# Performance work log

Measured on AMD Instinct MI355X. Metric: run time of the kernel, lower is better.

Reference implementation:

```python
import jax, jax.numpy as jnp
import numpy as np

B, S, F, H, T = 1024, 64, 2, 128, 24  # batch, src_len, n_features, hidden, output_length


def setup_inputs() -> dict:
    key = jax.random.key(0)
    ks = jax.random.split(key, 20)
    def p(k, shape):
        return jax.random.normal(k, shape, jnp.float32) * 0.05
    return {
        "x": jax.random.normal(ks[0], (B, S, F), jnp.float32),
        "prev_y": jnp.zeros((B, F), jnp.float32),
        # encoder 3-layer LSTM (PyTorch gate order i,f,g,o; b = b_ih + b_hh fused)
        "enc_Wih0": p(ks[1], (4 * H, F)),
        "enc_Whh0": p(ks[2], (4 * H, H)),
        "enc_b0": p(ks[3], (4 * H,)),
        "enc_Wih12": p(ks[4], (2, 4 * H, H)),
        "enc_Whh12": p(ks[5], (2, 4 * H, H)),
        "enc_b12": p(ks[6], (2, 4 * H)),
        # Bahdanau attention
        "attn_W": p(ks[7], (H, 2 * H)),
        "attn_b": p(ks[8], (H,)),
        "v_W": p(ks[9], (H,)),
        # decoder 3-layer LSTM, input size H+2
        "dec_Wih0": p(ks[10], (4 * H, H + 2)),
        "dec_Whh0": p(ks[11], (4 * H, H)),
        "dec_b0": p(ks[12], (4 * H,)),
        "dec_Wih12": p(ks[13], (2, 4 * H, H)),
        "dec_Whh12": p(ks[14], (2, 4 * H, H)),
        "dec_b12": p(ks[15], (2, 4 * H)),
        # output head Linear(2H, 2)
        "out_W": p(ks[16], (2, 2 * H)),
        "out_b": p(ks[17], (2,)),
    }


def _lstm_cell(xt, h, c, Wih, Whh, b):
    g = xt @ Wih.T + h @ Whh.T + b  # [B, 4H]
    i, f, gg, o = jnp.split(g, 4, axis=-1)
    c = jax.nn.sigmoid(f) * c + jax.nn.sigmoid(i) * jnp.tanh(gg)
    h = jax.nn.sigmoid(o) * jnp.tanh(c)
    return h, c


def _lstm_layer(xs, Wih, Whh, b):
    # xs: [S, B, in] -> hs [S, B, H], final (h, c)
    z = jnp.zeros((xs.shape[1], Whh.shape[1]), xs.dtype)
    def step(carry, xt):
        h, c = _lstm_cell(xt, carry[0], carry[1], Wih, Whh, b)
        return (h, c), h
    (hT, cT), hs = jax.lax.scan(step, (z, z), xs)
    return hs, hT, cT


def reference(x, prev_y, enc_Wih0, enc_Whh0, enc_b0, enc_Wih12, enc_Whh12, enc_b12,
              attn_W, attn_b, v_W, dec_Wih0, dec_Whh0, dec_b0, dec_Wih12, dec_Whh12,
              dec_b12, out_W, out_b):
    # ---- encoder: 3-layer LSTM over time ----
    hs, h0, c0 = _lstm_layer(jnp.swapaxes(x, 0, 1), enc_Wih0, enc_Whh0, enc_b0)
    hid, cel = [h0], [c0]
    for l in range(2):
        hs, hT, cT = _lstm_layer(hs, enc_Wih12[l], enc_Whh12[l], enc_b12[l])
        hid.append(hT); cel.append(cT)
    enc_out = jnp.swapaxes(hs, 0, 1)            # [B, S, H]
    h = jnp.stack(hid)                           # [3, B, H]
    c = jnp.stack(cel)

    def dec_step(carry, _):
        prev_out, h, c = carry
        h_top = h[2]                                             # top-layer hidden [B, H]
        a_in = jnp.concatenate(
            [jnp.broadcast_to(h_top[:, None, :], enc_out.shape), enc_out], axis=-1)  # [B, S, 2H]
        scores = jnp.tanh(a_in @ attn_W.T + attn_b) @ v_W        # [B, S]
        attw = jax.nn.softmax(scores, axis=1)
        weighted = jnp.einsum('bs,bsd->bd', attw, enc_out)        # [B, H]
        rnn_in = jnp.concatenate([prev_out, weighted], axis=-1)   # [B, H+2]
        h0n, c0n = _lstm_cell(rnn_in, h[0], c[0], dec_Wih0, dec_Whh0, dec_b0)
        h1n, c1n = _lstm_cell(h0n, h[1], c[1], dec_Wih12[0], dec_Whh12[0], dec_b12[0])
        h2n, c2n = _lstm_cell(h1n, h[2], c[2], dec_Wih12[1], dec_Whh12[1], dec_b12[1])
        out = jnp.concatenate([h2n, weighted], axis=-1) @ out_W.T + out_b  # [B, 2]
        return (out, jnp.stack([h0n, h1n, h2n]), jnp.stack([c0n, c1n, c2n])), out

    _, outs = jax.lax.scan(dec_step, (prev_y, h, c), None, length=T)
    return outs  # [T, B, 2]
```

## Files before the change

### kernel.cpp

```cpp
#include <hip/hip_runtime.h>
#include <hip/hip_fp16.h>

#define SEQ   64
#define HID   128
#define TOUT  24

typedef unsigned int u32;
typedef _Float16 f16;
typedef __attribute__((ext_vector_type(8))) f16 f16x8;
typedef __attribute__((ext_vector_type(4))) float f32x4;
#define MFMA __builtin_amdgcn_mfma_f32_16x16x32_f16

static __device__ __forceinline__ float sigm(float x){
  return __builtin_amdgcn_rcpf(1.f + __expf(-x));
}
static __device__ __forceinline__ float tanh_fast(float x){
  return fmaf(2.f, __builtin_amdgcn_rcpf(1.f + __expf(-2.f*x)), -1.f);
}

__global__ void prep_kernel(
    const float* __restrict__ eWih0,  const float* __restrict__ eWhh0,
    const float* __restrict__ eWih12, const float* __restrict__ eWhh12,
    const float* __restrict__ aW,
    const float* __restrict__ dWih0,  const float* __restrict__ dWhh0,
    const float* __restrict__ dWih12, const float* __restrict__ dWhh12,
    const float* __restrict__ oW,
    __half* __restrict__ wE0, __half* __restrict__ wE1, __half* __restrict__ wE2,
    __half* __restrict__ wD0, __half* __restrict__ wD1, __half* __restrict__ wD2,
    __half* __restrict__ wAh, __half* __restrict__ wAeF, float* __restrict__ wOT,
    float* __restrict__ dW2)
{
  int id = blockIdx.x*blockDim.x + threadIdx.x;
  if (id < 65536){
    int m=id, jj=m&7, l=(m>>3)&63, kt=(m>>9)&3, nt=m>>11;
    int col = nt*16 + (l&15), k = kt*32 + ((l>>4)<<3) + jj;
    wE0[m] = __float2half(eWhh0[col*128 + k]); return;
  }
  id -= 65536;
  if (id < 5*131072){
    int seg = id >> 17, m = id & 131071;
    int jj=m&7, l=(m>>3)&63, kt=(m>>9)&7, nt=m>>12;
    int col = nt*16 + (l&15), k = kt*32 + ((l>>4)<<3) + jj;
    float v;
    if (seg==0)      v = (k<128)? eWih12[col*128+k]         : eWhh12[col*128 + (k-128)];
    else if (seg==1) v = (k<128)? eWih12[65536+col*128+k]   : eWhh12[65536 + col*128 + (k-128)];
    else if (seg==2) v = (k<128)? dWih0[col*130 + 2 + k]    : dWhh0[col*128 + (k-128)];
    else if (seg==3) v = (k<128)? dWih12[col*128+k]         : dWhh12[col*128 + (k-128)];
    else             v = (k<128)? dWih12[65536+col*128+k]   : dWhh12[65536 + col*128 + (k-128)];
    __half hv = __float2half(v);
    if (seg==0){ wE1[m] = hv; return; }
    if (seg==1){ wE2[m] = hv; return; }
    __half* dst = (seg==2)? wD0 : (seg==3)? wD1 : wD2;
#pragma unroll
    for (int c=0; c<4; ++c) dst[(size_t)c*131072 + m] = hv;
    return;
  }
  id -= 5*131072;
  if (id < 16384){
    int m=id, jj=m&7, l=(m>>3)&63, kt=(m>>9)&3, nt=m>>11;
    int col = nt*16 + (l&15), k = kt*32 + ((l>>4)<<3) + jj;
    __half hv = __float2half(aW[col*256 + k]);
#pragma unroll
    for (int c=0; c<4; ++c) wAh[(size_t)c*16384 + m] = hv;
    return;
  }
  id -= 16384;
  if (id < 16384){
    int m=id, jj=m&7, l=(m>>3)&63, kt=(m>>9)&3, nt=m>>11;
    int col = nt*16 + (l&15), k = kt*32 + ((l>>4)<<3) + jj;
    wAeF[m] = __float2half(aW[col*256 + 128 + k]); return;
  }
  id -= 16384;
  if (id < 512){ int k=id>>1, jo=id&1; wOT[id] = oW[jo*256 + k]; return; }
  id -= 512;
  if (id < 1024){ int col=id>>1, ki=id&1; dW2[id] = dWih0[col*130 + ki]; return; }
}

__global__ __launch_bounds__(512) __attribute__((amdgpu_waves_per_eu(2, 2)))
void enc_kernel(
    const float* __restrict__ x, const float* __restrict__ eb0,
    const float* __restrict__ eb12, const float* __restrict__ eWih0,
    const __half* __restrict__ wE0, const __half* __restrict__ wE1,
    const __half* __restrict__ wE2,
    __half* __restrict__ hs0, __half* __restrict__ hs1,
    __half* __restrict__ carryH, float* __restrict__ carryC)
{
  __shared__ __align__(16) __half hT[2][2048];

  const int tid = threadIdx.x, w = tid>>6, lane = tid&63;
  const int l15 = lane&15, g4 = lane>>4;
  const int j = w*16 + l15;
  const int b16 = blockIdx.x*16;
  const int K0 = ((j>>5)*64 + ((j>>3)&3)*16)*8 + (j&7);

  __half* hs0b = hs0 + (size_t)blockIdx.x*131072;
  __half* hs1b = hs1 + (size_t)blockIdx.x*131072;

  for (int layer=0; layer<3; ++layer){
    const __half* W  = (layer==0)? wE0 : (layer==1)? wE1 : wE2;
    const float* bs  = (layer==0)? eb0 : (layer==1)? eb12 : (eb12+512);
    const __half* hinb  = (layer==1)? hs0b : hs1b;
    __half* houtb = (layer==0)? hs0b : (layer==1)? hs1b : nullptr;

    float bias[4];
#pragma unroll
    for (int g=0; g<4; ++g) bias[g] = bs[g*128 + j];
    float2 wx[4];
    if (layer==0){
#pragma unroll
      for (int g=0; g<4; ++g) wx[g] = *(const float2*)(eWih0 + (g*128+j)*2);
    }
    const f16x8* wb = (const f16x8*)W + lane;
    f16x8 Wh[16];
    if (layer==0){
#pragma unroll
      for (int g=0; g<4; ++g)
#pragma unroll
        for (int kt=0; kt<4; ++kt) Wh[g*4+kt] = wb[(size_t)((g*8+w)*4 + kt)*64];
    } else {
#pragma unroll
      for (int g=0; g<4; ++g)
#pragma unroll
        for (int kt=0; kt<4; ++kt) Wh[g*4+kt] = wb[(size_t)((g*8+w)*8 + 4 + kt)*64];
    }
    float c[4] = {0.f,0.f,0.f,0.f};
    ((u32*)hT[0])[tid] = 0u; ((u32*)hT[0])[tid+512] = 0u;
    __syncthreads();

    float2 xv[4]; f16x8 alo[4];
    if (layer==0){
#pragma unroll
      for (int q=0; q<4; ++q) xv[q] = *(const float2*)(x + ((size_t)(b16+g4*4+q)*SEQ + 0)*2);
    } else {
#pragma unroll
      for (int kt=0; kt<4; ++kt) alo[kt] = *(const f16x8*)(hinb + (kt*64+lane)*8);
    }

    int cur = 0;
    for (int t=0; t<SEQ; ++t){
      f16x8 wi[16];
      if (layer>0){
#pragma unroll
        for (int g=0; g<4; ++g)
#pragma unroll
          for (int kt=0; kt<4; ++kt) wi[g*4+kt] = wb[(size_t)((g*8+w)*8 + kt)*64];
      }
      f16x8 ah[4];
#pragma unroll
      for (int kt=0; kt<4; ++kt) ah[kt] = *(const f16x8*)(hT[cur] + (kt*64+lane)*8);
      float2 xcur[4]; f16x8 acur[4];
      if (layer==0){
#pragma unroll
        for (int q=0; q<4; ++q) xcur[q] = xv[q];
        if (t+1 < SEQ)
#pragma unroll
          for (int q=0; q<4; ++q) xv[q] = *(const float2*)(x + ((size_t)(b16+g4*4+q)*SEQ + t+1)*2);
      } else {
#pragma unroll
        for (int kt=0; kt<4; ++kt) acur[kt] = alo[kt];
        if (t+1 < SEQ)
#pragma unroll
          for (int kt=0; kt<4; ++kt) alo[kt] = *(const f16x8*)(hinb + (size_t)(t+1)*2048 + (kt*64+lane)*8);
      }
      f32x4 acc[4];
#pragma unroll
      for (int g=0; g<4; ++g) acc[g] = (f32x4){0.f,0.f,0.f,0.f};
#pragma unroll
      for (int g=0; g<4; ++g)
#pragma unroll
        for (int kt=0; kt<4; ++kt) acc[g] = MFMA(ah[kt], Wh[g*4+kt], acc[g], 0,0,0);
      if (layer>0){
#pragma unroll
        for (int g=0; g<4; ++g)
#pragma unroll
          for (int kt=0; kt<4; ++kt) acc[g] = MFMA(acur[kt], wi[g*4+kt], acc[g], 0,0,0);
      }
#pragma unroll
      for (int q=0; q<4; ++q){
        float gi = acc[0][q]+bias[0], gf = acc[1][q]+bias[1],
              gg = acc[2][q]+bias[2], go = acc[3][q]+bias[3];
        if (layer==0){
          gi += xcur[q].x*wx[0].x + xcur[q].y*wx[0].y;
          gf += xcur[q].x*wx[1].x + xcur[q].y*wx[1].y;
          gg += xcur[q].x*wx[2].x + xcur[q].y*wx[2].y;
          go += xcur[q].x*wx[3].x + xcur[q].y*wx[3].y;
        }
        float cn = fmaf(sigm(gf), c[q], sigm(gi)*tanh_fast(gg));
        float hn = sigm(go)*tanh_fast(cn);
        c[q] = cn;
        __half hh = __float2half(hn);
        hT[cur^1][K0 + (g4*4+q)*8] = hh;
        if (layer < 2){
          houtb[(size_t)t*2048 + K0 + (g4*4+q)*8] = hh;
        } else {
          int off = g4*32768 + q*8192 + (t>>4)*2048 + (j>>5)*512
                  + ((t&15) + ((j>>3)&3)*16)*8 + (j&7);
          hs0b[off] = hh;
        }
        if (t == SEQ-1){
          int ci = (layer*1024 + b16 + g4*4 + q)*128 + j;
          carryH[ci] = hh;
          carryC[ci] = cn;
        }
      }
      __syncthreads();
      cur ^= 1;
    }
    __syncthreads();
  }
}

#define LDQ(Q, g, kh) \
  Q[0] = wb[(size_t)((g)*64 + (kh)*4 + 0)*64]; \
  Q[1] = wb[(size_t)((g)*64 + (kh)*4 + 1)*64]; \
  Q[2] = wb[(size_t)((g)*64 + (kh)*4 + 2)*64]; \
  Q[3] = wb[(size_t)((g)*64 + (kh)*4 + 3)*64];
#define MM4(Q, A, g) \
  acc[g] = MFMA(A[0], Q[0], acc[g], 0,0,0); \
  acc[g] = MFMA(A[1], Q[1], acc[g], 0,0,0); \
  acc[g] = MFMA(A[2], Q[2], acc[g], 0,0,0); \
  acc[g] = MFMA(A[3], Q[3], acc[g], 0,0,0);

static __device__ __forceinline__ void dec_gemm(const __half* __restrict__ W,
    const __half* __restrict__ A0, const __half* __restrict__ A1,
    f32x4* acc, int lane, int w8)
{
  const f16x8* wb = (const f16x8*)W + (size_t)(w8*8)*64 + lane;
  f16x8 qA[4], qB[4], a0[4], a1[4];
  LDQ(qA, 0, 0)
  LDQ(qB, 1, 0)
#pragma unroll
  for (int kt=0; kt<4; ++kt) a0[kt] = *(const f16x8*)(A0 + (kt*64+lane)*8);
#pragma unroll
  for (int g=0; g<4; ++g) acc[g] = (f32x4){0.f,0.f,0.f,0.f};
  MM4(qA, a0, 0)  LDQ(qA, 2, 0)
  MM4(qB, a0, 1)  LDQ(qB, 3, 0)
#pragma unroll
  for (int kt=0; kt<4; ++kt) a1[kt] = *(const f16x8*)(A1 + (kt*64+lane)*8);
  MM4(qA, a0, 2)  LDQ(qA, 0, 1)
  MM4(qB, a0, 3)  LDQ(qB, 1, 1)
  MM4(qA, a1, 0)  LDQ(qA, 2, 1)
  MM4(qB, a1, 1)  LDQ(qB, 3, 1)
  MM4(qA, a1, 2)
  MM4(qB, a1, 3)
}

__global__ __launch_bounds__(512)
void dec_kernel(
    const float* __restrict__ prev_y, const float* __restrict__ db0,
    const float* __restrict__ db12, const float* __restrict__ ob,
    const float* __restrict__ ab, const float* __restrict__ vW,
    const __half* __restrict__ wD0, const __half* __restrict__ wD1,
    const __half* __restrict__ wD2, const __half* __restrict__ wAh,
    const __half* __restrict__ wAeF, const float* __restrict__ wOT,
    const float* __restrict__ dW2, const __half* __restrict__ encAg,
    const __half* __restrict__ carryH, const float* __restrict__ carryC,
    float* __restrict__ dout)
{
  __shared__ __align__(16) __half hT[4][2048];
  __shared__ float hp[4][132];
  __shared__ float scbF[256];
  __shared__ __align__(16) __half scb16h[256];
  __shared__ float po[4][2];
  __shared__ float vwl[128];
  extern __shared__ __align__(16) __half dyn[];
  __half* encBL = dyn;
  __half* epL   = dyn + 32768;

  const int tid = threadIdx.x, w = tid>>6, lane = tid&63;
  const int l15 = lane&15, g4 = lane>>4;
  const int d = blockIdx.x, b4 = d*4;
  const int w8 = (w + d) & 7;
  const int j = w8*16 + l15;
  const int K0 = ((j>>5)*64 + ((j>>3)&3)*16)*8 + (j&7);
  const __half* encAd = encAg + (size_t)(d>>2)*131072 + (size_t)(d&3)*32768;
  const int cp = (d>>3)&3;
  const __half* wD0d = wD0 + (size_t)cp*131072;
  const __half* wD1d = wD1 + (size_t)cp*131072;
  const __half* wD2d = wD2 + (size_t)cp*131072;
  const __half* wAhd = wAh + (size_t)cp*16384;

  float cD[3][4];
  if (g4 == 0){
#pragma unroll
    for (int l=0; l<3; ++l)
#pragma unroll
      for (int q=0; q<4; ++q){
        int ci = (l*1024 + b4 + q)*128 + j;
        hT[1+l][K0 + q*8] = carryH[ci];
        cD[l][q] = carryC[ci];
      }
  }
  if (tid < 8) po[tid>>1][tid&1] = prev_y[(b4 + (tid>>1))*2 + (tid&1)];
  if (tid < 128) vwl[tid] = vW[tid];

#pragma unroll
  for (int it=0; it<8; ++it){
    int lin = it*512 + tid;
    f16x8 v = *(const f16x8*)(encAd + (size_t)lin*8);
    int laneA = lin&63, ktA = (lin>>6)&3, sb = (lin>>8)&3, r4 = (lin>>10)&3;
    int s  = sb*16 + (laneA&15);
    int d0 = ktA*32 + ((laneA>>4)<<3);
    int base = r4*8192 + ((d0>>4)*2 + (s>>5))*512 + (s&7);
    int lb0  = (d0&15) + ((s>>3)&3)*16;
    f16* eb = (f16*)encBL;
#pragma unroll
    for (int u=0; u<8; ++u) eb[base + (lb0+u)*8] = v[u];
  }
#pragma unroll
  for (int i=0; i<2; ++i){
    int mt = w*2 + i, r4 = mt>>2, sb = mt&3;
    f16x8 a[4];
#pragma unroll
    for (int kt=0; kt<4; ++kt)
      a[kt] = *(const f16x8*)(encAd + (size_t)(((r4*4+sb)*4 + kt)*64 + lane)*8);
    const f16x8* bw = (const f16x8*)wAeF + lane;
#pragma unroll
    for (int nt=0; nt<8; ++nt){
      int col = nt*16 + l15;
      float abv = ab[col];
      f32x4 acc = {abv, abv, abv, abv};
#pragma unroll
      for (int kt=0; kt<4; ++kt) acc = MFMA(a[kt], bw[(size_t)(nt*4+kt)*64], acc, 0,0,0);
      int srow = r4*64 + sb*16 + g4*4;
#pragma unroll
      for (int q=0; q<4; ++q) epL[(srow+q)*132 + col] = __float2half(acc[q]);
    }
  }
  __syncthreads();

  auto cell = [&](float* crl, const float* bdp, const float* dwp, __half* hdst,
                  const f32x4* acc){
    float b0 = bdp[j], b1 = bdp[128+j], b2 = bdp[256+j], b3 = bdp[384+j];
    float2 w0, w1, w2, w3;
    if (dwp){
      w0 = *(const float2*)(dwp + 2*j);
      w1 = *(const float2*)(dwp + 2*(128+j));
      w2 = *(const float2*)(dwp + 2*(256+j));
      w3 = *(const float2*)(dwp + 2*(384+j));
    }
#pragma unroll
    for (int q=0; q<4; ++q){
      float gi = acc[0][q]+b0, gf = acc[1][q]+b1, gg = acc[2][q]+b2, go = acc[3][q]+b3;
      if (dwp){
        float p0 = po[q][0], p1 = po[q][1];
        gi += p0*w0.x + p1*w0.y;
        gf += p0*w1.x + p1*w1.y;
        gg += p0*w2.x + p1*w2.y;
        go += p0*w3.x + p1*w3.y;
      }
      float cn = fmaf(sigm(gf), crl[q], sigm(gi)*tanh_fast(gg));
      float hn = sigm(go)*tanh_fast(cn);
      crl[q] = cn;
      hdst[K0 + q*8] = __float2half(hn);
    }
  };

  int zr = 0;
  for (int t=0; t<TOUT; ++t){
    asm volatile("" : "+v"(zr));
    const float*  db0t  = db0  + zr;
    const float*  db12t = db12 + zr;
    const float*  dW2t  = dW2  + zr;
    const __half* wAht  = wAhd + zr;

    {
      f16x8 a[4], wAhR[4];
      const f16x8* wbh = (const f16x8*)wAht + lane;
#pragma unroll
      for (int kt=0; kt<4; ++kt) wAhR[kt] = wbh[(size_t)(w8*4+kt)*64];
#pragma unroll
      for (int kt=0; kt<4; ++kt) a[kt] = *(const f16x8*)(hT[3] + (kt*64+lane)*8);
      f32x4 acc = {0.f,0.f,0.f,0.f};
#pragma unroll
      for (int kt=0; kt<4; ++kt) acc = MFMA(a[kt], wAhR[kt], acc, 0,0,0);
      if (g4 == 0){
#pragma unroll
        for (int q=0; q<4; ++q) hp[q][j] = acc[q];
      }
    }
    __syncthreads();
    {
      int rs = tid>>1, r = rs>>6, jh = tid&1;
      const __half* er = epL + rs*132 + jh*64;
      const float* hr = hp[r] + jh*64;
      const float* vr = vwl + jh*64;
      float sc = 0.f;
#pragma unroll
      for (int p=0; p<8; ++p){
        f16x8 e = *(const f16x8*)(er + p*8);
#pragma unroll
        for (int u=0; u<8; ++u)
          sc = fmaf(tanh_fast((float)e[u] + hr[p*8+u]), vr[p*8+u], sc);
      }
      sc += __shfl_xor(sc, 1);
      if (jh == 0) scbF[rs] = sc;
    }
    __syncthreads();
    if (tid < 256){
      float v = scbF[tid];
      float m = v;
#pragma unroll
      for (int off=32; off; off>>=1) m = fmaxf(m, __shfl_xor(m, off));
      float e = __expf(v - m);
      float sm = e;
#pragma unroll
      for (int off=32; off; off>>=1) sm += __shfl_xor(sm, off);
      scb16h[tid] = __float2half(e * __builtin_amdgcn_rcpf(sm));
    }
    __syncthreads();
    {
#pragma unroll
      for (int r=0; r<4; ++r){
        f32x4 acc = {0.f,0.f,0.f,0.f};
#pragma unroll
        for (int kt=0; kt<2; ++kt){
          f16x8 abc = *(const f16x8*)(scb16h + r*64 + kt*32 + g4*8);
          f16x8 b   = *(const f16x8*)(encBL + r*8192 + ((w8*2+kt)*64 + lane)*8);
          acc = MFMA(abc, b, acc, 0,0,0);
        }
        if (lane < 16) hT[0][K0 + r*8] = __float2half(acc[0]);
      }
    }
    __syncthreads();
    f32x4 acc[4];
    dec_gemm(wD0d, hT[0], hT[1], acc, lane, w8);
    if (g4 == 0) cell(cD[0], db0t, dW2t, hT[1], acc);
    __syncthreads();
    dec_gemm(wD1d, hT[1], hT[2], acc, lane, w8);
    if (g4 == 0) cell(cD[1], db12t, nullptr, hT[2], acc);
    __syncthreads();
    dec_gemm(wD2d, hT[2], hT[3], acc, lane, w8);
    if (g4 == 0) cell(cD[2], db12t + 512, nullptr, hT[3], acc);
    __syncthreads();
    if (tid < 256){
      int r = tid>>6, kl = tid&63;
      int k2 = kl*2;
      int sl = ((k2>>5)*64 + r + ((k2>>3)&3)*16)*8 + (k2&7);
      float2 h2f = __half22float2(*(const __half2*)(hT[3] + sl));
      float2 wwf = __half22float2(*(const __half2*)(hT[0] + sl));
      float2 a0 = *(const float2*)(wOT + k2*2);
      float2 a1 = *(const float2*)(wOT + k2*2 + 2);
      float2 b0v = *(const float2*)(wOT + (128+k2)*2);
      float2 b1v = *(const float2*)(wOT + (128+k2)*2 + 2);
      float o0 = h2f.x*a0.x + h2f.y*a1.x + wwf.x*b0v.x + wwf.y*b1v.x;
      float o1 = h2f.x*a0.y + h2f.y*a1.y + wwf.x*b0v.y + wwf.y*b1v.y;
#pragma unroll
      for (int off=32; off; off>>=1){ o0 += __shfl_xor(o0, off); o1 += __shfl_xor(o1, off); }
      if (kl == 0){
        float v0 = o0 + ob[0], v1 = o1 + ob[1];
        size_t oi = ((size_t)t*1024 + b4 + r)*2;
        dout[oi] = v0; dout[oi+1] = v1;
        po[r][0] = v0; po[r][1] = v1;
      }
    }
  }
}

extern "C" void kernel_launch(void* const* d_in, const int* in_sizes, int n_in,
                              void* d_out, int out_size, void* d_ws, size_t ws_size,
                              hipStream_t stream) {
  const float* x      = (const float*)d_in[0];
  const float* prev_y = (const float*)d_in[1];
  const float* eWih0  = (const float*)d_in[2];
  const float* eWhh0  = (const float*)d_in[3];
  const float* eb0    = (const float*)d_in[4];
  const float* eWih12 = (const float*)d_in[5];
  const float* eWhh12 = (const float*)d_in[6];
  const float* eb12   = (const float*)d_in[7];
  const float* aW     = (const float*)d_in[8];
  const float* ab     = (const float*)d_in[9];
  const float* vW     = (const float*)d_in[10];
  const float* dWih0  = (const float*)d_in[11];
  const float* dWhh0  = (const float*)d_in[12];
  const float* db0    = (const float*)d_in[13];
  const float* dWih12 = (const float*)d_in[14];
  const float* dWhh12 = (const float*)d_in[15];
  const float* db12   = (const float*)d_in[16];
  const float* oW     = (const float*)d_in[17];
  const float* ob     = (const float*)d_in[18];

  __half* wE0  = (__half*)d_ws;
  __half* wE1  = wE0 + 65536;
  __half* wE2  = wE1 + 131072;
  __half* wD0  = wE2 + 131072;
  __half* wD1  = wD0 + 4*131072;
  __half* wD2  = wD1 + 4*131072;
  __half* wAh  = wD2 + 4*131072;
  __half* wAeF = wAh + 4*16384;
  float*  wOT  = (float*)(wAeF + 16384);
  float*  dW2  = wOT + 512;
  __half* hs0  = (__half*)(dW2 + 1024);
  __half* hs1  = hs0 + (size_t)64*131072;
  __half* carryH = hs1 + (size_t)64*131072;
  float*  carryC = (float*)(carryH + 393216);

  const int prepN = 65536 + 5*131072 + 16384 + 16384 + 512 + 1024;
  prep_kernel<<<(prepN + 255)/256, 256, 0, stream>>>(
      eWih0, eWhh0, eWih12, eWhh12, aW, dWih0, dWhh0, dWih12, dWhh12, oW,
      wE0, wE1, wE2, wD0, wD1, wD2, wAh, wAeF, wOT, dW2);

  enc_kernel<<<64, 512, 0, stream>>>(
      x, eb0, eb12, eWih0, wE0, wE1, wE2, hs0, hs1, carryH, carryC);

  const int dynB = (32768 + 256*132) * 2;
  hipFuncSetAttribute(reinterpret_cast<const void*>(dec_kernel),
                      hipFuncAttributeMaxDynamicSharedMemorySize, dynB);
  dec_kernel<<<256, 512, dynB, stream>>>(
      prev_y, db0, db12, ob, ab, vW, wD0, wD1, wD2, wAh, wAeF, wOT, dW2,
      hs0, carryH, carryC, (float*)d_out);
}
```

Baseline: 749.7 us.

## Split encoder gates across 16 waves and stage gate preactivations in LDS

The encoder now launches 1024 threads per block instead of 512. Each wave computes two 16-column gate tiles, keeps both the recurrent and input weight fragments in registers, and writes preactivations to shared memory. A barrier follows, then each thread applies the LSTM cell for two hidden units of one batch row. This is meant to halve the per-wave MFMA chain length and stop reloading input weights from global memory every timestep, at the cost of an extra barrier and an LDS round trip per step. Separately, the decoder weight copies are reduced from four replicas to two, which cuts prep-kernel writes but may increase cache contention in the decoder.

New measurement: 686.3 us. -8.5%, faster.

```diff
diff --git a/kernel.cpp b/kernel.cpp
--- a/kernel.cpp
+++ b/kernel.cpp
@@ -51,8 +51,7 @@
     if (seg==0){ wE1[m] = hv; return; }
     if (seg==1){ wE2[m] = hv; return; }
     __half* dst = (seg==2)? wD0 : (seg==3)? wD1 : wD2;
-#pragma unroll
-    for (int c=0; c<4; ++c) dst[(size_t)c*131072 + m] = hv;
+    dst[m] = hv; dst[131072 + m] = hv;
     return;
   }
   id -= 5*131072;
@@ -60,8 +59,7 @@
     int m=id, jj=m&7, l=(m>>3)&63, kt=(m>>9)&3, nt=m>>11;
     int col = nt*16 + (l&15), k = kt*32 + ((l>>4)<<3) + jj;
     __half hv = __float2half(aW[col*256 + k]);
-#pragma unroll
-    for (int c=0; c<4; ++c) wAh[(size_t)c*16384 + m] = hv;
+    wAh[m] = hv; wAh[16384 + m] = hv;
     return;
   }
   id -= 16384;
@@ -76,8 +74,7 @@
   if (id < 1024){ int col=id>>1, ki=id&1; dW2[id] = dWih0[col*130 + ki]; return; }
 }
 
-__global__ __launch_bounds__(512) __attribute__((amdgpu_waves_per_eu(2, 2)))
-void enc_kernel(
+__global__ __launch_bounds__(1024) void enc_kernel(
     const float* __restrict__ x, const float* __restrict__ eb0,
     const float* __restrict__ eb12, const float* __restrict__ eWih0,
     const __half* __restrict__ wE0, const __half* __restrict__ wE1,
@@ -86,12 +83,14 @@
     __half* __restrict__ carryH, float* __restrict__ carryC)
 {
   __shared__ __align__(16) __half hT[2][2048];
+  __shared__ __align__(16) float gpre[16*516];
+  __shared__ float xc[2][16][2];
 
   const int tid = threadIdx.x, w = tid>>6, lane = tid&63;
   const int l15 = lane&15, g4 = lane>>4;
-  const int j = w*16 + l15;
   const int b16 = blockIdx.x*16;
-  const int K0 = ((j>>5)*64 + ((j>>3)&3)*16)*8 + (j&7);
+  const int rp = tid>>6;
+  const int c0 = tid&63;
 
   __half* hs0b = hs0 + (size_t)blockIdx.x*131072;
   __half* hs1b = hs1 + (size_t)blockIdx.x*131072;
@@ -99,106 +98,106 @@
   for (int layer=0; layer<3; ++layer){
     const __half* W  = (layer==0)? wE0 : (layer==1)? wE1 : wE2;
     const float* bs  = (layer==0)? eb0 : (layer==1)? eb12 : (eb12+512);
-    const __half* hinb  = (layer==1)? hs0b : hs1b;
+    const __half* hinb = (layer==1)? hs0b : hs1b;
     __half* houtb = (layer==0)? hs0b : (layer==1)? hs1b : nullptr;
 
-    float bias[4];
-#pragma unroll
-    for (int g=0; g<4; ++g) bias[g] = bs[g*128 + j];
-    float2 wx[4];
+    float bias[4][2];
+#pragma unroll
+    for (int g=0; g<4; ++g){
+      bias[g][0] = bs[g*128 + c0];
+      bias[g][1] = bs[g*128 + c0 + 64];
+    }
+    float2 wx[4][2];
     if (layer==0){
 #pragma unroll
-      for (int g=0; g<4; ++g) wx[g] = *(const float2*)(eWih0 + (g*128+j)*2);
+      for (int g=0; g<4; ++g){
+        wx[g][0] = *(const float2*)(eWih0 + (g*128 + c0)*2);
+        wx[g][1] = *(const float2*)(eWih0 + (g*128 + c0 + 64)*2);
+      }
     }
     const f16x8* wb = (const f16x8*)W + lane;
-    f16x8 Wh[16];
+    f16x8 Wh[2][4], Wi[2][4];
     if (layer==0){
 #pragma unroll
-      for (int g=0; g<4; ++g)
-#pragma unroll
-        for (int kt=0; kt<4; ++kt) Wh[g*4+kt] = wb[(size_t)((g*8+w)*4 + kt)*64];
+      for (int n2=0; n2<2; ++n2)
+#pragma unroll
+        for (int kt=0; kt<4; ++kt) Wh[n2][kt] = wb[(size_t)((2*w+n2)*4 + kt)*64];
     } else {
 #pragma unroll
-      for (int g=0; g<4; ++g)
-#pragma unroll
-        for (int kt=0; kt<4; ++kt) Wh[g*4+kt] = wb[(size_t)((g*8+w)*8 + 4 + kt)*64];
-    }
-    float c[4] = {0.f,0.f,0.f,0.f};
-    ((u32*)hT[0])[tid] = 0u; ((u32*)hT[0])[tid+512] = 0u;
-    __syncthreads();
-
-    float2 xv[4]; f16x8 alo[4];
-    if (layer==0){
-#pragma unroll
-      for (int q=0; q<4; ++q) xv[q] = *(const float2*)(x + ((size_t)(b16+g4*4+q)*SEQ + 0)*2);
-    } else {
-#pragma unroll
-      for (int kt=0; kt<4; ++kt) alo[kt] = *(const f16x8*)(hinb + (kt*64+lane)*8);
-    }
+      for (int n2=0; n2<2; ++n2)
+#pragma unroll
+        for (int kt=0; kt<4; ++kt){
+          Wh[n2][kt] = wb[(size_t)((2*w+n2)*8 + 4 + kt)*64];
+          Wi[n2][kt] = wb[(size_t)((2*w+n2)*8 + kt)*64];
+        }
+    }
+    float c2[2] = {0.f, 0.f};
+    ((u32*)hT[0])[tid] = 0u;
+    if (layer==0 && tid < 32)
+      xc[0][tid>>1][tid&1] = x[((size_t)(b16 + (tid>>1))*SEQ + 0)*2 + (tid&1)];
+    __syncthreads();
 
     int cur = 0;
     for (int t=0; t<SEQ; ++t){
-      f16x8 wi[16];
+      f16x8 ah[4];
+#pragma unroll
+      for (int kt=0; kt<4; ++kt) ah[kt] = *(const f16x8*)(hT[cur] + (kt*64+lane)*8);
+      f32x4 acc[2];
+#pragma unroll
+      for (int n2=0; n2<2; ++n2) acc[n2] = (f32x4){0.f,0.f,0.f,0.f};
+#pragma unroll
+      for (int n2=0; n2<2; ++n2)
+#pragma unroll
+        for (int kt=0; kt<4; ++kt) acc[n2] = MFMA(ah[kt], Wh[n2][kt], acc[n2], 0,0,0);
       if (layer>0){
-#pragma unroll
-        for (int g=0; g<4; ++g)
-#pragma unroll
-          for (int kt=0; kt<4; ++kt) wi[g*4+kt] = wb[(size_t)((g*8+w)*8 + kt)*64];
-      }
-      f16x8 ah[4];
-#pragma unroll
-      for (int kt=0; kt<4; ++kt) ah[kt] = *(const f16x8*)(hT[cur] + (kt*64+lane)*8);
-      float2 xcur[4]; f16x8 acur[4];
-      if (layer==0){
-#pragma unroll
-        for (int q=0; q<4; ++q) xcur[q] = xv[q];
-        if (t+1 < SEQ)
-#pragma unroll
-          for (int q=0; q<4; ++q) xv[q] = *(const float2*)(x + ((size_t)(b16+g4*4+q)*SEQ + t+1)*2);
-      } else {
-#pragma unroll
-        for (int kt=0; kt<4; ++kt) acur[kt] = alo[kt];
-        if (t+1 < SEQ)
-#pragma unroll
-          for (int kt=0; kt<4; ++kt) alo[kt] = *(const f16x8*)(hinb + (size_t)(t+1)*2048 + (kt*64+lane)*8);
-      }
-      f32x4 acc[4];
-#pragma unroll
-      for (int g=0; g<4; ++g) acc[g] = (f32x4){0.f,0.f,0.f,0.f};
-#pragma unroll
-      for (int g=0; g<4; ++g)
-#pragma unroll
-        for (int kt=0; kt<4; ++kt) acc[g] = MFMA(ah[kt], Wh[g*4+kt], acc[g], 0,0,0);
-      if (layer>0){
-#pragma unroll
-        for (int g=0; g<4; ++g)
-#pragma unroll
-          for (int kt=0; kt<4; ++kt) acc[g] = MFMA(acur[kt], wi[g*4+kt], acc[g], 0,0,0);
-      }
-#pragma unroll
-      for (int q=0; q<4; ++q){
-        float gi = acc[0][q]+bias[0], gf = acc[1][q]+bias[1],
-              gg = acc[2][q]+bias[2], go = acc[3][q]+bias[3];
+        f16x8 acur[4];
+#pragma unroll
+        for (int kt=0; kt<4; ++kt)
+          acur[kt] = *(const f16x8*)(hinb + (size_t)t*2048 + (kt*64+lane)*8);
+#pragma unroll
+        for (int n2=0; n2<2; ++n2)
+#pragma unroll
+          for (int kt=0; kt<4; ++kt) acc[n2] = MFMA(acur[kt], Wi[n2][kt], acc[n2], 0,0,0);
+      }
+      if (layer==0 && tid < 32 && t+1 < SEQ)
+        xc[(t+1)&1][tid>>1][tid&1] = x[((size_t)(b16 + (tid>>1))*SEQ + t+1)*2 + (tid&1)];
+#pragma unroll
+      for (int n2=0; n2<2; ++n2)
+#pragma unroll
+        for (int q=0; q<4; ++q)
+          gpre[(g4*4+q)*516 + (2*w+n2)*16 + l15] = acc[n2][q];
+      __syncthreads();
+      float xv0 = 0.f, xv1 = 0.f;
+      if (layer==0){ xv0 = xc[t&1][rp][0]; xv1 = xc[t&1][rp][1]; }
+#pragma unroll
+      for (int u=0; u<2; ++u){
+        int cc = c0 + u*64;
+        const float* gp = gpre + rp*516 + cc;
+        float gi = gp[0]   + bias[0][u];
+        float gf = gp[128] + bias[1][u];
+        float gg = gp[256] + bias[2][u];
+        float go = gp[384] + bias[3][u];
         if (layer==0){
-          gi += xcur[q].x*wx[0].x + xcur[q].y*wx[0].y;
-          gf += xcur[q].x*wx[1].x + xcur[q].y*wx[1].y;
-          gg += xcur[q].x*wx[2].x + xcur[q].y*wx[2].y;
-          go += xcur[q].x*wx[3].x + xcur[q].y*wx[3].y;
+          gi += xv0*wx[0][u].x + xv1*wx[0][u].y;
+          gf += xv0*wx[1][u].x + xv1*wx[1][u].y;
+          gg += xv0*wx[2][u].x + xv1*wx[2][u].y;
+          go += xv0*wx[3][u].x + xv1*wx[3][u].y;
         }
-        float cn = fmaf(sigm(gf), c[q], sigm(gi)*tanh_fast(gg));
+        float cn = fmaf(sigm(gf), c2[u], sigm(gi)*tanh_fast(gg));
         float hn = sigm(go)*tanh_fast(cn);
-        c[q] = cn;
+        c2[u] = cn;
         __half hh = __float2half(hn);
-        hT[cur^1][K0 + (g4*4+q)*8] = hh;
+        int slot = ((cc>>5)*64 + rp + ((cc>>3)&3)*16)*8 + (cc&7);
+        hT[cur^1][slot] = hh;
         if (layer < 2){
-          houtb[(size_t)t*2048 + K0 + (g4*4+q)*8] = hh;
+          houtb[(size_t)t*2048 + slot] = hh;
         } else {
-          int off = g4*32768 + q*8192 + (t>>4)*2048 + (j>>5)*512
-                  + ((t&15) + ((j>>3)&3)*16)*8 + (j&7);
+          int off = (rp>>2)*32768 + (rp&3)*8192 + (t>>4)*2048 + (cc>>5)*512
+                  + ((t&15) + ((cc>>3)&3)*16)*8 + (cc&7);
           hs0b[off] = hh;
         }
         if (t == SEQ-1){
-          int ci = (layer*1024 + b16 + g4*4 + q)*128 + j;
+          int ci = (layer*1024 + b16 + rp)*128 + cc;
           carryH[ci] = hh;
           carryC[ci] = cn;
         }
@@ -274,7 +273,7 @@
   const int j = w8*16 + l15;
   const int K0 = ((j>>5)*64 + ((j>>3)&3)*16)*8 + (j&7);
   const __half* encAd = encAg + (size_t)(d>>2)*131072 + (size_t)(d&3)*32768;
-  const int cp = (d>>3)&3;
+  const int cp = (d>>3)&1;
   const __half* wD0d = wD0 + (size_t)cp*131072;
   const __half* wD1d = wD1 + (size_t)cp*131072;
   const __half* wD2d = wD2 + (size_t)cp*131072;
@@ -484,10 +483,10 @@
   __half* wE1  = wE0 + 65536;
   __half* wE2  = wE1 + 131072;
   __half* wD0  = wE2 + 131072;
-  __half* wD1  = wD0 + 4*131072;
-  __half* wD2  = wD1 + 4*131072;
-  __half* wAh  = wD2 + 4*131072;
-  __half* wAeF = wAh + 4*16384;
+  __half* wD1  = wD0 + 2*131072;
+  __half* wD2  = wD1 + 2*131072;
+  __half* wAh  = wD2 + 2*131072;
+  __half* wAeF = wAh + 2*16384;
   float*  wOT  = (float*)(wAeF + 16384);
   float*  dW2  = wOT + 512;
   __half* hs0  = (__half*)(dW2 + 1024);
@@ -500,7 +499,7 @@
       eWih0, eWhh0, eWih12, eWhh12, aW, dWih0, dWhh0, dWih12, dWhh12, oW,
       wE0, wE1, wE2, wD0, wD1, wD2, wAh, wAeF, wOT, dW2);
 
-  enc_kernel<<<64, 512, 0, stream>>>(
+  enc_kernel<<<64, 1024, 0, stream>>>(
       x, eb0, eb12, eWih0, wE0, wE1, wE2, hs0, hs1, carryH, carryC);
 
   const int dynB = (32768 + 256*132) * 2;
```
